# Performance work log

Measured on AMD Instinct MI355X. Metric: run time of the kernel, lower is better.

The kernel has to match this reference:

```python
import jax, jax.numpy as jnp
import numpy as np

MODES = 4
WIDTH = 8
IN_CH = 3
OUT_CH = 6
LAMBDA_RES = 0.3


def spectral_conv3d(x, w1, w2, w3, w4):
    # x: [B, C, D, H, W] real. Standard FNO3d SpectralConv3d:
    # rfftn over last 3 dims, multiply low modes in 4 corner octants, irfftn.
    B, C, D, H, W = x.shape
    m = MODES
    x_ft = jnp.fft.rfftn(x, axes=(-3, -2, -1))  # [B,C,D,H,W//2+1] complex

    def mul(blk, w):
        return jnp.einsum('bixyz,ioxyz->boxyz', blk, w)

    out_ft = jnp.zeros((B, w1.shape[1], D, H, W // 2 + 1), dtype=x_ft.dtype)
    out_ft = out_ft.at[:, :, :m, :m, :m].set(mul(x_ft[:, :, :m, :m, :m], w1))
    out_ft = out_ft.at[:, :, -m:, :m, :m].set(mul(x_ft[:, :, -m:, :m, :m], w2))
    out_ft = out_ft.at[:, :, :m, -m:, :m].set(mul(x_ft[:, :, :m, -m:, :m], w3))
    out_ft = out_ft.at[:, :, -m:, -m:, :m].set(mul(x_ft[:, :, -m:, -m:, :m], w4))
    return jnp.fft.irfftn(out_ft, s=(D, H, W), axes=(-3, -2, -1))


def fno3d(u, fc0_w, fc0_b, spec_ws, conv_ws, conv_bs, fc1_w, fc1_b, fc2_w, fc2_b):
    # Lift: 1x1 conv via einsum (channels-first)
    x = jnp.einsum('bcdhw,oc->bodhw', u, fc0_w) + fc0_b[None, :, None, None, None]
    for i in range(4):
        w1, w2, w3, w4 = spec_ws[i]
        x1 = spectral_conv3d(x, w1, w2, w3, w4)
        x2 = jnp.einsum('bcdhw,oc->bodhw', x, conv_ws[i]) + conv_bs[i][None, :, None, None, None]
        x = x1 + x2
        if i < 3:
            x = jax.nn.gelu(x)
    x = jnp.einsum('bcdhw,oc->bodhw', x, fc1_w) + fc1_b[None, :, None, None, None]
    x = jax.nn.gelu(x)
    x = jnp.einsum('bcdhw,oc->bodhw', x, fc2_w) + fc2_b[None, :, None, None, None]
    return x


def setup_inputs() -> dict:
    key = jax.random.key(0)
    ks = jax.random.split(key, 32)
    B, D, H, W = 8, 64, 64, 64
    m, wd = MODES, WIDTH
    u = jax.random.normal(ks[0], (B, IN_CH, D, H, W), dtype=jnp.float32)
    scale = 1.0 / (wd * wd)
    spec_ws = []
    ki = 1
    for _ in range(4):
        layer = []
        for _ in range(4):
            re = jax.random.uniform(ks[ki], (wd, wd, m, m, m)) * scale
            im = jax.random.uniform(ks[ki + 1], (wd, wd, m, m, m)) * scale
            layer.append(re + 1j * im)
            ki += 2
        spec_ws.append(tuple(layer))
    conv_ws = [jax.random.normal(ks[ki + i], (wd, wd)) * (1.0 / wd) for i in range(4)]
    ki += 4
    conv_bs = [jnp.zeros((wd,), jnp.float32) for _ in range(4)]
    fc0_w = jax.random.normal(ks[ki], (wd, IN_CH)) * 0.3; ki += 1
    fc0_b = jnp.zeros((wd,), jnp.float32)
    fc1_w = jax.random.normal(ks[ki], (4 * wd, wd)) * 0.2; ki += 1
    fc1_b = jnp.zeros((4 * wd,), jnp.float32)
    fc2_w = jax.random.normal(ks[ki], (OUT_CH, 4 * wd)) * 0.2; ki += 1
    fc2_b = jnp.zeros((OUT_CH,), jnp.float32)
    nu = jnp.asarray(0.001, jnp.float32)
    return {
        'u': u, 'nu': nu,
        'fc0_w': fc0_w, 'fc0_b': fc0_b,
        'spec_ws': spec_ws, 'conv_ws': conv_ws, 'conv_bs': conv_bs,
        'fc1_w': fc1_w, 'fc1_b': fc1_b, 'fc2_w': fc2_w, 'fc2_b': fc2_b,
    }


def reference(u, nu, fc0_w, fc0_b, spec_ws, conv_ws, conv_bs, fc1_w, fc1_b, fc2_w, fc2_b):
    B, C, D, H, W = u.shape
    # hard core: zeros [B,6,D,H,W] with first 3 channels = u*nu
    hard = jnp.concatenate([u * nu, jnp.zeros((B, 3, D, H, W), u.dtype)], axis=1)
    soft = fno3d(u, fc0_w, fc0_b, spec_ws, conv_ws, conv_bs, fc1_w, fc1_b, fc2_w, fc2_b)
    return hard + LAMBDA_RES * soft
```

## Files before the change

### kernel.cpp

```cpp
#include <hip/hip_runtime.h>


#define TWO_PI_OVER_64 0.09817477042468103

__device__ __forceinline__ float gelu_fast(float x) {
    float x2 = x * x;
    float p  = x * (1.0f + 0.044715f * x2);
    float e  = __builtin_amdgcn_exp2f(-2.3022083f * p);
    return x * __builtin_amdgcn_rcpf(1.0f + e);
}

#define BUILD_TW() \
    __shared__ float twc[64], tws[64]; \
    if (threadIdx.x < 64) { \
        double a_ = TWO_PI_OVER_64 * (double)threadIdx.x; \
        twc[threadIdx.x] = (float)cos(a_); tws[threadIdx.x] = (float)sin(a_); \
    }

__device__ __forceinline__ void a_tail_store(
    const float v[4], const float c1[4], const float s1[4],
    const float c2[4], const float s2[4], const float c3[4], const float s3[4],
    int wq, float2* __restrict__ Arow)
{
    float p0  = v[0] + v[1] + v[2] + v[3];
    float ar1 = v[0]*c1[0] + v[1]*c1[1] + v[2]*c1[2] + v[3]*c1[3];
    float ai1 = -(v[0]*s1[0] + v[1]*s1[1] + v[2]*s1[2] + v[3]*s1[3]);
    float ar2 = v[0]*c2[0] + v[1]*c2[1] + v[2]*c2[2] + v[3]*c2[3];
    float ai2 = -(v[0]*s2[0] + v[1]*s2[1] + v[2]*s2[2] + v[3]*s2[3]);
    float ar3 = v[0]*c3[0] + v[1]*c3[1] + v[2]*c3[2] + v[3]*c3[3];
    float ai3 = -(v[0]*s3[0] + v[1]*s3[1] + v[2]*s3[2] + v[3]*s3[3]);
    #pragma unroll
    for (int m = 1; m < 16; m <<= 1) {
        p0  += __shfl_xor(p0,  m);
        ar1 += __shfl_xor(ar1, m);  ai1 += __shfl_xor(ai1, m);
        ar2 += __shfl_xor(ar2, m);  ai2 += __shfl_xor(ai2, m);
        ar3 += __shfl_xor(ar3, m);  ai3 += __shfl_xor(ai3, m);
    }
    if (wq < 2) {
        float4 av;
        av.x = (wq == 0) ? p0   : ar2;
        av.y = (wq == 0) ? 0.f  : ai2;
        av.z = (wq == 0) ? ar1  : ar3;
        av.w = (wq == 0) ? ai1  : ai3;
        *((float4*)Arow + wq) = av;
    }
}

__global__ __launch_bounds__(256) void k_liftA(
    const float* __restrict__ u, const float* __restrict__ fc0w,
    const float* __restrict__ fc0b, float* __restrict__ x,
    float2* __restrict__ A)
{
    BUILD_TW();
    const int t = threadIdx.x, bid = blockIdx.x;
    const int b = bid >> 8, dx = (bid >> 2) & 63, dy0 = (bid & 3) * 16;
    const int dyl = t >> 4, wq = t & 15;
    const size_t sp = (size_t)dx * 4096 + (size_t)(dy0 + dyl) * 64 + wq * 4;
    float uin[3][4];
    #pragma unroll
    for (int c = 0; c < 3; ++c) {
        float4 v = *(const float4*)&u[(size_t)(b * 3 + c) * 262144 + sp];
        uin[c][0] = v.x; uin[c][1] = v.y; uin[c][2] = v.z; uin[c][3] = v.w;
    }
    __syncthreads();
    float c1[4], s1[4], c2[4], s2[4], c3[4], s3[4];
    #pragma unroll
    for (int j = 0; j < 4; ++j) {
        int w = wq * 4 + j;
        c1[j] = twc[w];             s1[j] = tws[w];
        c2[j] = twc[(2 * w) & 63];  s2[j] = tws[(2 * w) & 63];
        c3[j] = twc[(3 * w) & 63];  s3[j] = tws[(3 * w) & 63];
    }
    #pragma unroll
    for (int o = 0; o < 8; ++o) {
        float w0 = fc0w[o * 3 + 0], w1 = fc0w[o * 3 + 1], w2 = fc0w[o * 3 + 2];
        float bb = fc0b[o];
        float v[4];
        #pragma unroll
        for (int j = 0; j < 4; ++j)
            v[j] = bb + uin[0][j] * w0 + uin[1][j] * w1 + uin[2][j] * w2;
        *(float4*)&x[(size_t)(b * 8 + o) * 262144 + sp] =
            make_float4(v[0], v[1], v[2], v[3]);
        a_tail_store(v, c1, s1, c2, s2, c3, s3, wq,
                     A + ((size_t)(b * 8 + o) * 4096 + dx * 64 + dy0 + dyl) * 4);
    }
}

__global__ __launch_bounds__(256) void k_fH(const float2* __restrict__ A,
                                            float2* __restrict__ Bh)
{
    BUILD_TW();
    __syncthreads();
    const int g = blockIdx.x * 256 + threadIdx.x;
    const int triple = g >> 5, idx = g & 31;
    const int ky = idx >> 2, kz = idx & 3;
    const int b = triple >> 9, c = (triple >> 6) & 7, dx = triple & 63;
    const int kyv = ky < 4 ? ky : ky + 56;
    const float2* Ap = A + (size_t)(b * 8 + c) * 16384 + dx * 256 + kz;
    float re = 0.f, im = 0.f;
    int ti = 0;
    #pragma unroll 8
    for (int dy = 0; dy < 64; ++dy) {
        float2 a = Ap[dy * 4];
        float cc = twc[ti], ss = tws[ti];
        re += a.x * cc + a.y * ss;
        im += a.y * cc - a.x * ss;
        ti = (ti + kyv) & 63;
    }
    Bh[(size_t)(b * 8 + c) * 2048 + dx * 32 + ky * 4 + kz] = make_float2(re, im);
}

__global__ __launch_bounds__(256) void k_fDmix(
    const float2* __restrict__ Bh,
    const float2* __restrict__ w1, const float2* __restrict__ w2,
    const float2* __restrict__ w3, const float2* __restrict__ w4,
    float2* __restrict__ O)
{
    BUILD_TW();
    __shared__ float2 Cs[256];
    const int t = threadIdx.x, bid = blockIdx.x;
    const int b = bid >> 3, kx = bid & 7;
    const int kxv = kx < 4 ? kx : kx + 56;
    __syncthreads();
    {
        int kz = t & 3, ky = (t >> 2) & 7, c = t >> 5;
        const float2* Bp = Bh + (size_t)(b * 8 + c) * 2048 + ky * 4 + kz;
        float re = 0.f, im = 0.f;
        int ti = 0;
        #pragma unroll 8
        for (int dx = 0; dx < 64; ++dx) {
            float2 v = Bp[dx * 32];
            float cc = twc[ti], ss = tws[ti];
            re += v.x * cc + v.y * ss;
            im += v.y * cc - v.x * ss;
            ti = (ti + kxv) & 63;
        }
        Cs[t] = make_float2(re, im);
    }
    __syncthreads();
    {
        int kz = t & 3, ky = (t >> 2) & 7, o = t >> 5;
        const float2* wsel = (kx < 4) ? ((ky < 4) ? w1 : w3) : ((ky < 4) ? w2 : w4);
        int kxw = kx & 3, kyw = ky & 3;
        float re = 0.f, im = 0.f;
        #pragma unroll
        for (int i = 0; i < 8; ++i) {
            float2 cv = Cs[i * 32 + ky * 4 + kz];
            float2 wv = wsel[(((size_t)(i * 8 + o) * 4 + kxw) * 4 + kyw) * 4 + kz];
            re += cv.x * wv.x - cv.y * wv.y;
            im += cv.x * wv.y + cv.y * wv.x;
        }
        O[(((size_t)(b * 8 + o) * 8 + kx) * 8 + ky) * 4 + kz] = make_float2(re, im);
    }
}

__global__ __launch_bounds__(256, 4) void k_ptA(
    float* __restrict__ x, const float2* __restrict__ O,
    const float* __restrict__ cw, const float* __restrict__ cb,
    float2* __restrict__ A)
{
    BUILD_TW();
    __shared__ float2 Ps[256];
    __shared__ float2 Qs[8 * 16 * 4];
    const int t = threadIdx.x, bid = blockIdx.x;
    const int b = bid >> 8, dx = (bid >> 2) & 63, dy0 = (bid & 3) * 16;
    const int dyl = t >> 4, wq = t & 15;
    const size_t sp = (size_t)dx * 4096 + (size_t)(dy0 + dyl) * 64 + wq * 4;
    float4 xv[8];
    #pragma unroll
    for (int c = 0; c < 8; ++c)
        xv[c] = *(const float4*)&x[(size_t)(b * 8 + c) * 262144 + sp];
    const int pkz = t & 3, pky = (t >> 2) & 7, po = t >> 5;
    float2 ov[8];
    #pragma unroll
    for (int kxi = 0; kxi < 8; ++kxi)
        ov[kxi] = O[(((size_t)(b * 8 + po) * 8 + kxi) * 8 + pky) * 4 + pkz];
    __syncthreads();
    {
        float re = 0.f, im = 0.f;
        #pragma unroll
        for (int kxi = 0; kxi < 8; ++kxi) {
            int kxv = kxi < 4 ? kxi : kxi + 56;
            int ti = (kxv * dx) & 63;
            float cc = twc[ti], ss = tws[ti];
            re += ov[kxi].x * cc - ov[kxi].y * ss;
            im += ov[kxi].y * cc + ov[kxi].x * ss;
        }
        Ps[t] = make_float2(re, im);
    }
    __syncthreads();
    for (int it = t; it < 512; it += 256) {
        int kz = it & 3, qdyl = (it >> 2) & 15, o = it >> 6;
        int dy = dy0 + qdyl;
        float re = 0.f, im = 0.f;
        #pragma unroll
        for (int kyi = 0; kyi < 8; ++kyi) {
            int kyv = kyi < 4 ? kyi : kyi + 56;
            int ti = (kyv * dy) & 63;
            float2 v = Ps[(o * 8 + kyi) * 4 + kz];
            float cc = twc[ti], ss = tws[ti];
            re += v.x * cc - v.y * ss;
            im += v.y * cc + v.x * ss;
        }
        Qs[(o * 16 + qdyl) * 4 + kz] = make_float2(re, im);
    }
    __syncthreads();
    float c1[4], s1[4], c2[4], s2[4], c3[4], s3[4];
    #pragma unroll
    for (int j = 0; j < 4; ++j) {
        int w = wq * 4 + j;
        c1[j] = twc[w];             s1[j] = tws[w];
        c2[j] = twc[(2 * w) & 63];  s2[j] = tws[(2 * w) & 63];
        c3[j] = twc[(3 * w) & 63];  s3[j] = tws[(3 * w) & 63];
    }
    const float invN3 = 1.0f / 262144.0f;
    #pragma unroll
    for (int o = 0; o < 8; ++o) {
        float4 qa = *(const float4*)&Qs[(o * 16 + dyl) * 4];
        float4 qb = *(const float4*)&Qs[(o * 16 + dyl) * 4 + 2];
        float outj[4];
        #pragma unroll
        for (int j = 0; j < 4; ++j) {
            float x1 = qa.x + 2.f * (qa.z * c1[j] - qa.w * s1[j]
                                   + qb.x * c2[j] - qb.y * s2[j]
                                   + qb.z * c3[j] - qb.w * s3[j]);
            x1 *= invN3;
            float x2 = cb[o];
            #pragma unroll
            for (int c = 0; c < 8; ++c) {
                const float* xc = &xv[c].x;
                x2 += cw[o * 8 + c] * xc[j];
            }
            outj[j] = gelu_fast(x1 + x2);
        }
        *(float4*)&x[(size_t)(b * 8 + o) * 262144 + sp] =
            make_float4(outj[0], outj[1], outj[2], outj[3]);
        a_tail_store(outj, c1, s1, c2, s2, c3, s3, wq,
                     A + ((size_t)(b * 8 + o) * 4096 + dx * 64 + dy0 + dyl) * 4);
    }
}

__global__ __launch_bounds__(256, 4) void k_ptout(
    const float* __restrict__ x, const float2* __restrict__ O,
    const float* __restrict__ cw, const float* __restrict__ cb,
    const float* __restrict__ u, const float* __restrict__ nu,
    const float* __restrict__ fc1w, const float* __restrict__ fc1b,
    const float* __restrict__ fc2w, const float* __restrict__ fc2b,
    float* __restrict__ out)
{
    BUILD_TW();
    __shared__ float2 Ps[256];
    __shared__ float2 Qs[8 * 16 * 4];
    const int t = threadIdx.x, bid = blockIdx.x;
    const int b = bid >> 8, dx = (bid >> 2) & 63, dy0 = (bid & 3) * 16;
    const int dyl = t >> 4, wq = t & 15;
    const size_t sp = (size_t)dx * 4096 + (size_t)(dy0 + dyl) * 64 + wq * 4;
    float4 xv[8];
    #pragma unroll
    for (int c = 0; c < 8; ++c)
        xv[c] = *(const float4*)&x[(size_t)(b * 8 + c) * 262144 + sp];
    float4 uv[3];
    #pragma unroll
    for (int c = 0; c < 3; ++c)
        uv[c] = *(const float4*)&u[(size_t)(b * 3 + c) * 262144 + sp];
    const int pkz = t & 3, pky = (t >> 2) & 7, po = t >> 5;
    float2 ovv[8];
    #pragma unroll
    for (int kxi = 0; kxi < 8; ++kxi)
        ovv[kxi] = O[(((size_t)(b * 8 + po) * 8 + kxi) * 8 + pky) * 4 + pkz];
    __syncthreads();
    {
        float re = 0.f, im = 0.f;
        #pragma unroll
        for (int kxi = 0; kxi < 8; ++kxi) {
            int kxv = kxi < 4 ? kxi : kxi + 56;
            int ti = (kxv * dx) & 63;
            float cc = twc[ti], ss = tws[ti];
            re += ovv[kxi].x * cc - ovv[kxi].y * ss;
            im += ovv[kxi].y * cc + ovv[kxi].x * ss;
        }
        Ps[t] = make_float2(re, im);
    }
    __syncthreads();
    for (int it = t; it < 512; it += 256) {
        int kz = it & 3, qdyl = (it >> 2) & 15, o = it >> 6;
        int dy = dy0 + qdyl;
        float re = 0.f, im = 0.f;
        #pragma unroll
        for (int kyi = 0; kyi < 8; ++kyi) {
            int kyv = kyi < 4 ? kyi : kyi + 56;
            int ti = (kyv * dy) & 63;
            float2 v = Ps[(o * 8 + kyi) * 4 + kz];
            float cc = twc[ti], ss = tws[ti];
            re += v.x * cc - v.y * ss;
            im += v.y * cc + v.x * ss;
        }
        Qs[(o * 16 + qdyl) * 4 + kz] = make_float2(re, im);
    }
    __syncthreads();
    float c1[4], s1[4], c2[4], s2[4], c3[4], s3[4];
    #pragma unroll
    for (int j = 0; j < 4; ++j) {
        int w = wq * 4 + j;
        c1[j] = twc[w];             s1[j] = tws[w];
        c2[j] = twc[(2 * w) & 63];  s2[j] = tws[(2 * w) & 63];
        c3[j] = twc[(3 * w) & 63];  s3[j] = tws[(3 * w) & 63];
    }
    const float invN3 = 1.0f / 262144.0f;
    float vv[8][4];
    #pragma unroll
    for (int o = 0; o < 8; ++o) {
        float4 qa = *(const float4*)&Qs[(o * 16 + dyl) * 4];
        float4 qb = *(const float4*)&Qs[(o * 16 + dyl) * 4 + 2];
        #pragma unroll
        for (int j = 0; j < 4; ++j) {
            float x1 = qa.x + 2.f * (qa.z * c1[j] - qa.w * s1[j]
                                   + qb.x * c2[j] - qb.y * s2[j]
                                   + qb.z * c3[j] - qb.w * s3[j]);
            x1 *= invN3;
            float x2 = cb[o];
            #pragma unroll
            for (int c = 0; c < 8; ++c) {
                const float* xc = &xv[c].x;
                x2 += cw[o * 8 + c] * xc[j];
            }
            vv[o][j] = x1 + x2;
        }
    }
    float so[6][4];
    #pragma unroll
    for (int c6 = 0; c6 < 6; ++c6)
        #pragma unroll
        for (int j = 0; j < 4; ++j) so[c6][j] = fc2b[c6];
    #pragma unroll 4
    for (int h = 0; h < 32; ++h) {
        float wr[8];
        #pragma unroll
        for (int c = 0; c < 8; ++c) wr[c] = fc1w[h * 8 + c];
        const float hb = fc1b[h];
        float w2r[6];
        #pragma unroll
        for (int c6 = 0; c6 < 6; ++c6) w2r[c6] = fc2w[c6 * 32 + h];
        #pragma unroll
        for (int j = 0; j < 4; ++j) {
            float a = hb;
            #pragma unroll
            for (int c = 0; c < 8; ++c) a += vv[c][j] * wr[c];
            float g = gelu_fast(a);
            #pragma unroll
            for (int c6 = 0; c6 < 6; ++c6) so[c6][j] += g * w2r[c6];
        }
    }
    const float nuv = nu[0];
    #pragma unroll
    for (int c6 = 0; c6 < 6; ++c6) {
        float4 res;
        float* rp = &res.x;
        if (c6 < 3) {
            const float* up = &uv[c6].x;
            #pragma unroll
            for (int j = 0; j < 4; ++j) rp[j] = 0.3f * so[c6][j] + up[j] * nuv;
        } else {
            #pragma unroll
            for (int j = 0; j < 4; ++j) rp[j] = 0.3f * so[c6][j];
        }
        *(float4*)&out[(size_t)(b * 6 + c6) * 262144 + sp] = res;
    }
}

__global__ void k_pack(const float* __restrict__ re, const float* __restrict__ im,
                       float2* __restrict__ dst)
{
    int i = blockIdx.x * 256 + threadIdx.x;
    if (i < 4096) dst[i] = make_float2(re[i], im[i]);
}

extern "C" void kernel_launch(void* const* d_in, const int* in_sizes, int n_in,
                              void* d_out, int out_size, void* d_ws, size_t ws_size,
                              hipStream_t stream)
{
    (void)out_size;
    const char* leaf[32];
    bool spec_split = false;
    const char* spec_re[16]; const char* spec_im[16];
    int src = 0;
    leaf[0] = (const char*)d_in[src++];
    leaf[1] = (const char*)d_in[src++];
    leaf[2] = (const char*)d_in[src++];
    leaf[3] = (const char*)d_in[src++];
    {
        int s = (src < n_in) ? in_sizes[src] : 4096;
        if (n_in >= 48 && s == 4096) {
            spec_split = true;
            for (int i = 0; i < 16; ++i) {
                spec_re[i] = (const char*)d_in[src++];
                spec_im[i] = (const char*)d_in[src++];
            }
        } else {
            int per;
            if (s == 4096 || s == 8192) per = 1;
            else if (s == 16384 || s == 32768) per = 4;
            else per = 16;
            for (int i = 0; i < 16; i += per) {
                const char* base = (const char*)d_in[src++];
                for (int j = 0; j < per; ++j) leaf[4 + i + j] = base + (size_t)j * 4096 * 8;
            }
        }
    }
    {
        int s = (src < n_in) ? in_sizes[src] : 64;
        if (s == 64) { for (int i = 0; i < 4; ++i) leaf[20 + i] = (const char*)d_in[src++]; }
        else { const char* base = (const char*)d_in[src++];
               for (int i = 0; i < 4; ++i) leaf[20 + i] = base + (size_t)i * 64 * 4; }
    }
    {
        int s = (src < n_in) ? in_sizes[src] : 8;
        if (s == 8) { for (int i = 0; i < 4; ++i) leaf[24 + i] = (const char*)d_in[src++]; }
        else { const char* base = (const char*)d_in[src++];
               for (int i = 0; i < 4; ++i) leaf[24 + i] = base + (size_t)i * 8 * 4; }
    }
    leaf[28] = (const char*)d_in[src++];
    leaf[29] = (const char*)d_in[src++];
    leaf[30] = (const char*)d_in[src++];
    leaf[31] = (const char*)d_in[src++];

    const float* u    = (const float*)leaf[0];
    const float* nu   = (const float*)leaf[1];
    const float* fc0w = (const float*)leaf[2];
    const float* fc0b = (const float*)leaf[3];
    const float* convw[4], *convb[4];
    for (int i = 0; i < 4; ++i) { convw[i] = (const float*)leaf[20 + i];
                                  convb[i] = (const float*)leaf[24 + i]; }
    const float* fc1w = (const float*)leaf[28];
    const float* fc1b = (const float*)leaf[29];
    const float* fc2w = (const float*)leaf[30];
    const float* fc2b = (const float*)leaf[31];

    const size_t szX = 67108864, szA = 8388608, szB = 1048576,
                 szO = 131072, szSP = 524288;
    char* ws = (char*)d_ws;
    float* xbuf = (float*)ws;
    float2 *Abuf, *Bbuf, *Obuf, *SP;
    if (ws_size >= szX + szA + szB + szO + szSP) {
        Abuf = (float2*)(ws + szX);
        Bbuf = (float2*)(ws + szX + szA);
        Obuf = (float2*)(ws + szX + szA + szB);
        SP   = (float2*)(ws + szX + szA + szB + szO);
    } else {
        Obuf = (float2*)(ws + szX);
        Abuf = (float2*)d_out;
        Bbuf = (float2*)((char*)d_out + szA);
        SP   = (float2*)((char*)d_out + szA + szB);
    }

    const float2* specw[16];
    if (spec_split) {
        for (int i = 0; i < 16; ++i) {
            hipLaunchKernelGGL(k_pack, dim3(16), dim3(256), 0, stream,
                               (const float*)spec_re[i], (const float*)spec_im[i],
                               SP + (size_t)i * 4096);
            specw[i] = SP + (size_t)i * 4096;
        }
    } else {
        for (int i = 0; i < 16; ++i) specw[i] = (const float2*)leaf[4 + i];
    }
    float* outp = (float*)d_out;

    hipLaunchKernelGGL(k_liftA, dim3(2048), dim3(256), 0, stream, u, fc0w, fc0b, xbuf, Abuf);
    for (int L = 0; L < 4; ++L) {
        hipLaunchKernelGGL(k_fH, dim3(512), dim3(256), 0, stream, Abuf, Bbuf);
        hipLaunchKernelGGL(k_fDmix, dim3(64), dim3(256), 0, stream,
                           Bbuf, specw[L*4+0], specw[L*4+1], specw[L*4+2], specw[L*4+3], Obuf);
        if (L < 3) {
            hipLaunchKernelGGL(k_ptA, dim3(2048), dim3(256), 0, stream,
                               xbuf, Obuf, convw[L], convb[L], Abuf);
        } else {
            hipLaunchKernelGGL(k_ptout, dim3(2048), dim3(256), 0, stream,
                               xbuf, Obuf, convw[3], convb[3], u, nu,
                               fc1w, fc1b, fc2w, fc2b, outp);
        }
    }
}
```

Before: 306.7 us.

## Fuse H-axis DFT into pointwise kernels via LDS and atomic partial sums

The W-axis partial DFT results are now kept in shared memory, and each block computes its 16-row partial H-axis DFT, accumulating into the B buffer with atomicAdd. This removes the separate k_fH kernel and the 8MB intermediate A buffer round-trip. The cost is a memset of B before each layer and contended float atomics. The final k_ptout kernel is also re-split to 2 elements per thread over twice as many blocks, and the occupancy hint in the launch bounds is dropped.

Measured after the change: 315.2 us. 1.03x slower.

```diff
diff --git a/kernel.cpp b/kernel.cpp
--- a/kernel.cpp
+++ b/kernel.cpp
@@ -17,10 +17,10 @@
         twc[threadIdx.x] = (float)cos(a_); tws[threadIdx.x] = (float)sin(a_); \
     }
 
-__device__ __forceinline__ void a_tail_store(
+__device__ __forceinline__ void a_tail_lds(
     const float v[4], const float c1[4], const float s1[4],
     const float c2[4], const float s2[4], const float c3[4], const float s3[4],
-    int wq, float2* __restrict__ Arow)
+    int wq, float4* __restrict__ AslRow)
 {
     float p0  = v[0] + v[1] + v[2] + v[3];
     float ar1 = v[0]*c1[0] + v[1]*c1[1] + v[2]*c1[2] + v[3]*c1[3];
@@ -42,16 +42,39 @@
         av.y = (wq == 0) ? 0.f  : ai2;
         av.z = (wq == 0) ? ar1  : ar3;
         av.w = (wq == 0) ? ai1  : ai3;
-        *((float4*)Arow + wq) = av;
-    }
+        AslRow[wq] = av;
+    }
+}
+
+__device__ __forceinline__ void h_partial_atomic(
+    const float2* __restrict__ Asl, const float* __restrict__ twc,
+    const float* __restrict__ tws, int t, int b, int dx, int dy0,
+    float2* __restrict__ Bh)
+{
+    const int kz = t & 3, ky = (t >> 2) & 7, o = t >> 5;
+    const int kyv = ky < 4 ? ky : ky + 56;
+    float re = 0.f, im = 0.f;
+    int ti = (kyv * dy0) & 63;
+    #pragma unroll
+    for (int dyl = 0; dyl < 16; ++dyl) {
+        float2 a = Asl[(o * 16 + dyl) * 4 + kz];
+        float cc = twc[ti], ss = tws[ti];
+        re += a.x * cc + a.y * ss;
+        im += a.y * cc - a.x * ss;
+        ti = (ti + kyv) & 63;
+    }
+    float* p = (float*)&Bh[(size_t)(b * 8 + o) * 2048 + dx * 32 + ky * 4 + kz];
+    atomicAdd(p, re);
+    atomicAdd(p + 1, im);
 }
 
 __global__ __launch_bounds__(256) void k_liftA(
     const float* __restrict__ u, const float* __restrict__ fc0w,
     const float* __restrict__ fc0b, float* __restrict__ x,
-    float2* __restrict__ A)
+    float2* __restrict__ Bh)
 {
     BUILD_TW();
+    __shared__ float4 Asl4[8 * 16 * 2];
     const int t = threadIdx.x, bid = blockIdx.x;
     const int b = bid >> 8, dx = (bid >> 2) & 63, dy0 = (bid & 3) * 16;
     const int dyl = t >> 4, wq = t & 15;
@@ -81,33 +104,10 @@
             v[j] = bb + uin[0][j] * w0 + uin[1][j] * w1 + uin[2][j] * w2;
         *(float4*)&x[(size_t)(b * 8 + o) * 262144 + sp] =
             make_float4(v[0], v[1], v[2], v[3]);
-        a_tail_store(v, c1, s1, c2, s2, c3, s3, wq,
-                     A + ((size_t)(b * 8 + o) * 4096 + dx * 64 + dy0 + dyl) * 4);
-    }
-}
-
-__global__ __launch_bounds__(256) void k_fH(const float2* __restrict__ A,
-                                            float2* __restrict__ Bh)
-{
-    BUILD_TW();
-    __syncthreads();
-    const int g = blockIdx.x * 256 + threadIdx.x;
-    const int triple = g >> 5, idx = g & 31;
-    const int ky = idx >> 2, kz = idx & 3;
-    const int b = triple >> 9, c = (triple >> 6) & 7, dx = triple & 63;
-    const int kyv = ky < 4 ? ky : ky + 56;
-    const float2* Ap = A + (size_t)(b * 8 + c) * 16384 + dx * 256 + kz;
-    float re = 0.f, im = 0.f;
-    int ti = 0;
-    #pragma unroll 8
-    for (int dy = 0; dy < 64; ++dy) {
-        float2 a = Ap[dy * 4];
-        float cc = twc[ti], ss = tws[ti];
-        re += a.x * cc + a.y * ss;
-        im += a.y * cc - a.x * ss;
-        ti = (ti + kyv) & 63;
-    }
-    Bh[(size_t)(b * 8 + c) * 2048 + dx * 32 + ky * 4 + kz] = make_float2(re, im);
+        a_tail_lds(v, c1, s1, c2, s2, c3, s3, wq, &Asl4[(o * 16 + dyl) * 2]);
+    }
+    __syncthreads();
+    h_partial_atomic((const float2*)Asl4, twc, tws, t, b, dx, dy0, Bh);
 }
 
 __global__ __launch_bounds__(256) void k_fDmix(
@@ -154,14 +154,15 @@
     }
 }
 
-__global__ __launch_bounds__(256, 4) void k_ptA(
+__global__ __launch_bounds__(256) void k_ptA(
     float* __restrict__ x, const float2* __restrict__ O,
     const float* __restrict__ cw, const float* __restrict__ cb,
-    float2* __restrict__ A)
+    float2* __restrict__ Bh)
 {
     BUILD_TW();
     __shared__ float2 Ps[256];
     __shared__ float2 Qs[8 * 16 * 4];
+    __shared__ float4 Asl4[8 * 16 * 2];
     const int t = threadIdx.x, bid = blockIdx.x;
     const int b = bid >> 8, dx = (bid >> 2) & 63, dy0 = (bid & 3) * 16;
     const int dyl = t >> 4, wq = t & 15;
@@ -235,12 +236,13 @@
         }
         *(float4*)&x[(size_t)(b * 8 + o) * 262144 + sp] =
             make_float4(outj[0], outj[1], outj[2], outj[3]);
-        a_tail_store(outj, c1, s1, c2, s2, c3, s3, wq,
-                     A + ((size_t)(b * 8 + o) * 4096 + dx * 64 + dy0 + dyl) * 4);
-    }
-}
-
-__global__ __launch_bounds__(256, 4) void k_ptout(
+        a_tail_lds(outj, c1, s1, c2, s2, c3, s3, wq, &Asl4[(o * 16 + dyl) * 2]);
+    }
+    __syncthreads();
+    h_partial_atomic((const float2*)Asl4, twc, tws, t, b, dx, dy0, Bh);
+}
+
+__global__ __launch_bounds__(256) void k_ptout(
     const float* __restrict__ x, const float2* __restrict__ O,
     const float* __restrict__ cw, const float* __restrict__ cb,
     const float* __restrict__ u, const float* __restrict__ nu,
@@ -250,19 +252,19 @@
 {
     BUILD_TW();
     __shared__ float2 Ps[256];
-    __shared__ float2 Qs[8 * 16 * 4];
+    __shared__ float2 Qs[8 * 8 * 4];
     const int t = threadIdx.x, bid = blockIdx.x;
-    const int b = bid >> 8, dx = (bid >> 2) & 63, dy0 = (bid & 3) * 16;
-    const int dyl = t >> 4, wq = t & 15;
-    const size_t sp = (size_t)dx * 4096 + (size_t)(dy0 + dyl) * 64 + wq * 4;
-    float4 xv[8];
+    const int b = bid >> 9, dx = (bid >> 3) & 63, dy0 = (bid & 7) * 8;
+    const int dyl = t >> 5, wp = t & 31;
+    const size_t sp = (size_t)dx * 4096 + (size_t)(dy0 + dyl) * 64 + wp * 2;
+    float2 xv[8];
     #pragma unroll
     for (int c = 0; c < 8; ++c)
-        xv[c] = *(const float4*)&x[(size_t)(b * 8 + c) * 262144 + sp];
-    float4 uv[3];
+        xv[c] = *(const float2*)&x[(size_t)(b * 8 + c) * 262144 + sp];
+    float2 uv[3];
     #pragma unroll
     for (int c = 0; c < 3; ++c)
-        uv[c] = *(const float4*)&u[(size_t)(b * 3 + c) * 262144 + sp];
+        uv[c] = *(const float2*)&u[(size_t)(b * 3 + c) * 262144 + sp];
     const int pkz = t & 3, pky = (t >> 2) & 7, po = t >> 5;
     float2 ovv[8];
     #pragma unroll
@@ -282,8 +284,8 @@
         Ps[t] = make_float2(re, im);
     }
     __syncthreads();
-    for (int it = t; it < 512; it += 256) {
-        int kz = it & 3, qdyl = (it >> 2) & 15, o = it >> 6;
+    {
+        int kz = t & 3, qdyl = (t >> 2) & 7, o = t >> 5;
         int dy = dy0 + qdyl;
         float re = 0.f, im = 0.f;
         #pragma unroll
@@ -295,25 +297,25 @@
             re += v.x * cc - v.y * ss;
             im += v.y * cc + v.x * ss;
         }
-        Qs[(o * 16 + qdyl) * 4 + kz] = make_float2(re, im);
-    }
-    __syncthreads();
-    float c1[4], s1[4], c2[4], s2[4], c3[4], s3[4];
-    #pragma unroll
-    for (int j = 0; j < 4; ++j) {
-        int w = wq * 4 + j;
+        Qs[(o * 8 + qdyl) * 4 + kz] = make_float2(re, im);
+    }
+    __syncthreads();
+    float c1[2], s1[2], c2[2], s2[2], c3[2], s3[2];
+    #pragma unroll
+    for (int j = 0; j < 2; ++j) {
+        int w = wp * 2 + j;
         c1[j] = twc[w];             s1[j] = tws[w];
         c2[j] = twc[(2 * w) & 63];  s2[j] = tws[(2 * w) & 63];
         c3[j] = twc[(3 * w) & 63];  s3[j] = tws[(3 * w) & 63];
     }
     const float invN3 = 1.0f / 262144.0f;
-    float vv[8][4];
+    float vv[8][2];
     #pragma unroll
     for (int o = 0; o < 8; ++o) {
-        float4 qa = *(const float4*)&Qs[(o * 16 + dyl) * 4];
-        float4 qb = *(const float4*)&Qs[(o * 16 + dyl) * 4 + 2];
-        #pragma unroll
-        for (int j = 0; j < 4; ++j) {
+        float4 qa = *(const float4*)&Qs[(o * 8 + dyl) * 4];
+        float4 qb = *(const float4*)&Qs[(o * 8 + dyl) * 4 + 2];
+        #pragma unroll
+        for (int j = 0; j < 2; ++j) {
             float x1 = qa.x + 2.f * (qa.z * c1[j] - qa.w * s1[j]
                                    + qb.x * c2[j] - qb.y * s2[j]
                                    + qb.z * c3[j] - qb.w * s3[j]);
@@ -327,11 +329,11 @@
             vv[o][j] = x1 + x2;
         }
     }
-    float so[6][4];
+    float so[6][2];
     #pragma unroll
     for (int c6 = 0; c6 < 6; ++c6)
         #pragma unroll
-        for (int j = 0; j < 4; ++j) so[c6][j] = fc2b[c6];
+        for (int j = 0; j < 2; ++j) so[c6][j] = fc2b[c6];
     #pragma unroll 4
     for (int h = 0; h < 32; ++h) {
         float wr[8];
@@ -342,7 +344,7 @@
         #pragma unroll
         for (int c6 = 0; c6 < 6; ++c6) w2r[c6] = fc2w[c6 * 32 + h];
         #pragma unroll
-        for (int j = 0; j < 4; ++j) {
+        for (int j = 0; j < 2; ++j) {
             float a = hb;
             #pragma unroll
             for (int c = 0; c < 8; ++c) a += vv[c][j] * wr[c];
@@ -354,17 +356,15 @@
     const float nuv = nu[0];
     #pragma unroll
     for (int c6 = 0; c6 < 6; ++c6) {
-        float4 res;
-        float* rp = &res.x;
+        float2 res;
         if (c6 < 3) {
-            const float* up = &uv[c6].x;
-            #pragma unroll
-            for (int j = 0; j < 4; ++j) rp[j] = 0.3f * so[c6][j] + up[j] * nuv;
+            res.x = 0.3f * so[c6][0] + uv[c6].x * nuv;
+            res.y = 0.3f * so[c6][1] + uv[c6].y * nuv;
         } else {
-            #pragma unroll
-            for (int j = 0; j < 4; ++j) rp[j] = 0.3f * so[c6][j];
-        }
-        *(float4*)&out[(size_t)(b * 6 + c6) * 262144 + sp] = res;
+            res.x = 0.3f * so[c6][0];
+            res.y = 0.3f * so[c6][1];
+        }
+        *(float2*)&out[(size_t)(b * 6 + c6) * 262144 + sp] = res;
     }
 }
 
@@ -436,21 +436,18 @@
     const float* fc2w = (const float*)leaf[30];
     const float* fc2b = (const float*)leaf[31];
 
-    const size_t szX = 67108864, szA = 8388608, szB = 1048576,
-                 szO = 131072, szSP = 524288;
+    const size_t szX = 67108864, szB = 1048576, szO = 131072, szSP = 524288;
     char* ws = (char*)d_ws;
     float* xbuf = (float*)ws;
-    float2 *Abuf, *Bbuf, *Obuf, *SP;
-    if (ws_size >= szX + szA + szB + szO + szSP) {
-        Abuf = (float2*)(ws + szX);
-        Bbuf = (float2*)(ws + szX + szA);
-        Obuf = (float2*)(ws + szX + szA + szB);
-        SP   = (float2*)(ws + szX + szA + szB + szO);
+    float2 *Bbuf, *Obuf, *SP;
+    if (ws_size >= szX + szB + szO + szSP) {
+        Bbuf = (float2*)(ws + szX);
+        Obuf = (float2*)(ws + szX + szB);
+        SP   = (float2*)(ws + szX + szB + szO);
     } else {
         Obuf = (float2*)(ws + szX);
-        Abuf = (float2*)d_out;
-        Bbuf = (float2*)((char*)d_out + szA);
-        SP   = (float2*)((char*)d_out + szA + szB);
+        Bbuf = (float2*)d_out;
+        SP   = (float2*)((char*)d_out + szB);
     }
 
     const float2* specw[16];
@@ -466,16 +463,17 @@
     }
     float* outp = (float*)d_out;
 
-    hipLaunchKernelGGL(k_liftA, dim3(2048), dim3(256), 0, stream, u, fc0w, fc0b, xbuf, Abuf);
+    hipMemsetAsync(Bbuf, 0, szB, stream);
+    hipLaunchKernelGGL(k_liftA, dim3(2048), dim3(256), 0, stream, u, fc0w, fc0b, xbuf, Bbuf);
     for (int L = 0; L < 4; ++L) {
-        hipLaunchKernelGGL(k_fH, dim3(512), dim3(256), 0, stream, Abuf, Bbuf);
         hipLaunchKernelGGL(k_fDmix, dim3(64), dim3(256), 0, stream,
                            Bbuf, specw[L*4+0], specw[L*4+1], specw[L*4+2], specw[L*4+3], Obuf);
         if (L < 3) {
+            hipMemsetAsync(Bbuf, 0, szB, stream);
             hipLaunchKernelGGL(k_ptA, dim3(2048), dim3(256), 0, stream,
-                               xbuf, Obuf, convw[L], convb[L], Abuf);
+                               xbuf, Obuf, convw[L], convb[L], Bbuf);
         } else {
-            hipLaunchKernelGGL(k_ptout, dim3(2048), dim3(256), 0, stream,
+            hipLaunchKernelGGL(k_ptout, dim3(4096), dim3(256), 0, stream,
                                xbuf, Obuf, convw[3], convb[3], u, nu,
                                fc1w, fc1b, fc2w, fc2b, outp);
         }
```
